# Optimization experiments

Hardware: AMD Instinct MI355X
Metric: run time of the kernel (lower is better)

Reference implementation:

```python
import jax, jax.numpy as jnp
import numpy as np

H_FEATS = 256

def setup_inputs() -> dict:
    key = jax.random.key(0)
    k1, k2, k3, k4, k5, k6, k7 = jax.random.split(key, 7)
    N, E, D = 100000, 500000, H_FEATS
    h = jax.random.normal(k1, (N, D), dtype=jnp.float32)
    src = jax.random.randint(k2, (E,), 0, N)
    dst = jax.random.randint(k3, (E,), 0, N)
    # Linear params (PyTorch default init: U(-1/sqrt(fan_in), 1/sqrt(fan_in)))
    b1_bound = 1.0 / np.sqrt(2 * D)
    b2_bound = 1.0 / np.sqrt(D)
    W1 = jax.random.uniform(k4, (2 * D, D), jnp.float32, -b1_bound, b1_bound)
    b1 = jax.random.uniform(k5, (D,), jnp.float32, -b1_bound, b1_bound)
    W2 = jax.random.uniform(k6, (D, 1), jnp.float32, -b2_bound, b2_bound)
    b2 = jax.random.uniform(k7, (1,), jnp.float32, -b2_bound, b2_bound)
    return {"h": h, "src": src, "dst": dst, "W1": W1, "b1": b1, "W2": W2, "b2": b2}

def reference(h, src, dst, W1, b1, W2, b2):
    # Gather per-edge source/destination node features and concat: [E, 2D]
    he = jnp.concatenate([h[src], h[dst]], axis=1)
    # Linear -> ReLU -> (dropout is identity in eval) -> Linear -> Sigmoid
    hid = jax.nn.relu(he @ W1 + b1)          # [E, D]
    score = jax.nn.sigmoid((hid @ W2 + b2).squeeze(1))  # [E]
    return score
```

## Files before the change

kernel.cpp:

```cpp
#include <hip/hip_runtime.h>
#include <math.h>


typedef __attribute__((ext_vector_type(8))) short short8;
typedef __attribute__((ext_vector_type(2))) float floatx2;
typedef __attribute__((ext_vector_type(4))) float floatx4;
typedef __attribute__((ext_vector_type(16))) float floatx16;

#define D_FEAT 256
#define EPW 16

__device__ __forceinline__ float bf2f(unsigned short u) {
    union { unsigned u32; float f; } v; v.u32 = ((unsigned)u) << 16; return v.f;
}
__device__ __forceinline__ float lo16(unsigned u) {
    union { unsigned u32; float f; } v; v.u32 = u << 16; return v.f;
}
__device__ __forceinline__ float hi16(unsigned u) {
    union { unsigned u32; float f; } v; v.u32 = u & 0xffff0000u; return v.f;
}
__device__ __forceinline__ unsigned short f2bf(float f) {
    union { float f; unsigned u32; } v; v.f = f;
    unsigned x = v.u32;
    return (unsigned short)((x + 0x7fffu + ((x >> 16) & 1u)) >> 16);
}
__device__ __forceinline__ float sigmoid_safe(float r) {
    r = fminf(fmaxf(r, -30.f), 30.f);
    return 1.f / (1.f + expf(-r));
}
__device__ __forceinline__ unsigned pack4_fp8(float a, float b, float c, float d) {
    int w = __builtin_amdgcn_cvt_pk_fp8_f32(a, b, 0, false);
    w = __builtin_amdgcn_cvt_pk_fp8_f32(c, d, w, true);
    return (unsigned)w;
}

__device__ __forceinline__ int probe_block(const unsigned short* __restrict__ h,
                                           int tid) {
    __shared__ int cnt_s[4];
    int c = 0;
    #pragma unroll
    for (int i = 0; i < 8; ++i) {
        unsigned e = (h[tid * 8 + i] >> 7) & 0xFF;
        c += (e >= 100 && e <= 140) ? 1 : 0;
    }
    #pragma unroll
    for (int off = 32; off > 0; off >>= 1)
        c += __shfl_xor(c, off);
    if ((tid & 63) == 0) cnt_s[tid >> 6] = c;
    __syncthreads();
    int s = cnt_s[0] + cnt_s[1] + cnt_s[2] + cnt_s[3];
    return (s >= 1843) ? 1 : 0;
}

__global__ __launch_bounds__(256) void probe_dtype(const unsigned short* __restrict__ h,
                                                   int* __restrict__ flag) {
    int isbf16 = probe_block(h, threadIdx.x);
    if (threadIdx.x == 0) flag[0] = isbf16;
}

__global__ __launch_bounds__(256) void build_wt(const unsigned short* __restrict__ h,
                                                const void* __restrict__ W1v,
                                                unsigned short* __restrict__ Wt,
                                                int* __restrict__ flag) {
    const int isbf16 = probe_block(h, threadIdx.x);
    if (blockIdx.x == 0 && threadIdx.x == 0) flag[0] = isbf16;
    int j = blockIdx.x, k = threadIdx.x;
    size_t idx = (j < 256) ? ((size_t)k * 256 + j) : ((size_t)(k + 256) * 256 + (j - 256));
    unsigned short v;
    if (isbf16) v = ((const unsigned short*)W1v)[idx];
    else        v = f2bf(((const float*)W1v)[idx]);
    Wt[(size_t)j * 256 + k] = v;
}

__global__ __launch_bounds__(512, 2) void gemm_pq(const void* __restrict__ hv,
                                                  const unsigned short* __restrict__ Wt,
                                                  unsigned char* __restrict__ PQ8,
                                                  int N, const int* __restrict__ flag) {
    const int isbf16 = flag[0];
    __shared__ unsigned short Bs[256][256];
    __shared__ unsigned short As[64][256];

    const int tid  = threadIdx.x;
    const int lane = tid & 63;
    const int wid  = tid >> 6;
    const int l32  = lane & 31;
    const int q2   = lane >> 5;

    {
        const int r = tid >> 1;
        const unsigned cbase = (tid & 1) * 256;
        const char* srcp = (const char*)Wt + (size_t)r * 512 + cbase;
        char* dstb = (char*)&Bs[0][0] + (unsigned)r * 512;
        const unsigned sw = ((unsigned)r & 31) << 4;
        #pragma unroll
        for (int i = 0; i < 16; ++i) {
            short8 v = *(const short8*)(srcp + i * 16);
            *(short8*)(dstb + ((cbase + i * 16) ^ sw)) = v;
        }
    }

    short8 breg[16];
    {
        const char* bp = (const char*)Wt + (size_t)(256 + wid * 32 + l32) * 512 + q2 * 16;
        #pragma unroll
        for (int ks = 0; ks < 16; ++ks)
            breg[ks] = *(const short8*)(bp + ks * 32);
    }

    const int ar = tid >> 3;
    const unsigned ac = (unsigned)(tid & 7) * 64;
    const unsigned aswz = ((unsigned)ar & 31) << 4;

    short8 pref[4];
    auto load_a = [&](int ms) {
        const int gm = ms * 64 + ar;
        if (isbf16) {
            #pragma unroll
            for (int j = 0; j < 4; ++j) {
                short8 v = {};
                if (gm < N)
                    v = *(const short8*)((const char*)hv + (size_t)gm * 512 + ac + j * 16);
                pref[j] = v;
            }
        } else {
            #pragma unroll
            for (int j = 0; j < 4; ++j) {
                short8 v = {};
                if (gm < N) {
                    const float* p = (const float*)hv + (size_t)gm * 256 + (ac + j * 16) / 2;
                    floatx4 f0 = *(const floatx4*)p;
                    floatx4 f1 = *(const floatx4*)(p + 4);
                    v[0] = (short)f2bf(f0.x); v[1] = (short)f2bf(f0.y);
                    v[2] = (short)f2bf(f0.z); v[3] = (short)f2bf(f0.w);
                    v[4] = (short)f2bf(f1.x); v[5] = (short)f2bf(f1.y);
                    v[6] = (short)f2bf(f1.z); v[7] = (short)f2bf(f1.w);
                }
                pref[j] = v;
            }
        }
    };

    const int NT = (N + 63) >> 6;
    const int GM = gridDim.x;
    if ((int)blockIdx.x < NT) load_a(blockIdx.x);

    for (int ms = blockIdx.x; ms < NT; ms += GM) {
        __syncthreads();
        {
            char* adst = (char*)&As[0][0] + (unsigned)ar * 512;
            #pragma unroll
            for (int j = 0; j < 4; ++j)
                *(short8*)(adst + ((ac + j * 16) ^ aswz)) = pref[j];
        }
        __syncthreads();

        const int msn = ms + GM;
        if (msn < NT) load_a(msn);

        floatx16 acc[2][2] = {};
        #pragma unroll
        for (int ks = 0; ks < 16; ++ks) {
            const unsigned cb = ((unsigned)(ks * 32 + q2 * 16)) ^ ((unsigned)l32 << 4);
            short8 a0 = *(const short8*)((const char*)&As[0][0] + (unsigned)l32 * 512 + cb);
            short8 a1 = *(const short8*)((const char*)&As[0][0] + (unsigned)(32 + l32) * 512 + cb);
            short8 bl = *(const short8*)((const char*)&Bs[0][0] + (unsigned)(wid * 32 + l32) * 512 + cb);
            acc[0][0] = __builtin_amdgcn_mfma_f32_32x32x16_bf16(bl,       a0, acc[0][0], 0, 0, 0);
            acc[1][0] = __builtin_amdgcn_mfma_f32_32x32x16_bf16(bl,       a1, acc[1][0], 0, 0, 0);
            acc[0][1] = __builtin_amdgcn_mfma_f32_32x32x16_bf16(breg[ks], a0, acc[0][1], 0, 0, 0);
            acc[1][1] = __builtin_amdgcn_mfma_f32_32x32x16_bf16(breg[ks], a1, acc[1][1], 0, 0, 0);
        }

        __syncthreads();
        {
            unsigned char* scr = (unsigned char*)&As[0][0];
            #pragma unroll
            for (int mi = 0; mi < 2; ++mi) {
                const unsigned row = (unsigned)(mi * 32 + l32);
                const unsigned rs = (row & 31) << 4;
                #pragma unroll
                for (int nb = 0; nb < 2; ++nb) {
                    const unsigned nbase = (unsigned)(nb * 256 + wid * 32 + 4 * q2);
                    #pragma unroll
                    for (int g = 0; g < 4; ++g) {
                        unsigned w = pack4_fp8(acc[mi][nb][4 * g + 0], acc[mi][nb][4 * g + 1],
                                               acc[mi][nb][4 * g + 2], acc[mi][nb][4 * g + 3]);
                        const unsigned col = nbase + 8 * g;
                        *(unsigned*)(scr + ((row * 512 + col) ^ rs)) = w;
                    }
                }
            }
        }
        __syncthreads();
        {
            const unsigned char* scr = (const unsigned char*)&As[0][0];
            const int gm = ms * 64 + ar;
            if (gm < N) {
                #pragma unroll
                for (int j = 0; j < 4; ++j) {
                    const unsigned col = ac + j * 16;
                    uint4 v = *(const uint4*)(scr + (((unsigned)ar * 512 + col) ^ aswz));
                    *(uint4*)(PQ8 + (size_t)gm * 512 + col) = v;
                }
            }
        }
    }
}

__global__ __launch_bounds__(256) void edge_score(const unsigned char* __restrict__ PQ8,
                                                  const int* __restrict__ src,
                                                  const int* __restrict__ dst,
                                                  const void* __restrict__ b1v,
                                                  const void* __restrict__ W2v,
                                                  const void* __restrict__ b2v,
                                                  void* __restrict__ outv,
                                                  int E, const int* __restrict__ flag) {
    const int isbf16 = flag[0];
    const int wave = threadIdx.x >> 6;
    const int lane = threadIdx.x & 63;
    const int e0 = (blockIdx.x * 4 + wave) * EPW;
    if (e0 >= E) return;
    const int l32 = lane & 31;
    const int par = lane >> 5;

    float bf[8], wf[8];
    if (isbf16) {
        const uint4 bvr = *(const uint4*)((const unsigned short*)b1v + l32 * 8);
        const uint4 wvr = *(const uint4*)((const unsigned short*)W2v + l32 * 8);
        bf[0] = lo16(bvr.x); bf[1] = hi16(bvr.x); bf[2] = lo16(bvr.y); bf[3] = hi16(bvr.y);
        bf[4] = lo16(bvr.z); bf[5] = hi16(bvr.z); bf[6] = lo16(bvr.w); bf[7] = hi16(bvr.w);
        wf[0] = lo16(wvr.x); wf[1] = hi16(wvr.x); wf[2] = lo16(wvr.y); wf[3] = hi16(wvr.y);
        wf[4] = lo16(wvr.z); wf[5] = hi16(wvr.z); wf[6] = lo16(wvr.w); wf[7] = hi16(wvr.w);
    } else {
        const float* bp = (const float*)b1v + l32 * 8;
        const float* wp = (const float*)W2v + l32 * 8;
        #pragma unroll
        for (int t = 0; t < 8; ++t) { bf[t] = bp[t]; wf[t] = wp[t]; }
    }
    float bias2;
    if (isbf16) bias2 = bf2f(((const unsigned short*)b2v)[0]);
    else        bias2 = ((const float*)b2v)[0];

    int nsrc[8], ndst[8];
    #pragma unroll
    for (int p = 0; p < 8; ++p) {
        int e = e0 + 2 * p + par; if (e >= E) e = E - 1;
        nsrc[p] = src[e];
        ndst[p] = dst[e];
    }
    uint2 rp[8], rq[8];
    #pragma unroll
    for (int p = 0; p < 8; ++p) {
        rp[p] = *(const uint2*)(PQ8 + (size_t)nsrc[p] * 512 + l32 * 8);
        rq[p] = *(const uint2*)(PQ8 + (size_t)ndst[p] * 512 + 256 + l32 * 8);
    }

    float res[8];
    #pragma unroll
    for (int p = 0; p < 8; ++p) {
        floatx2 p01 = __builtin_amdgcn_cvt_pk_f32_fp8((int)rp[p].x, false);
        floatx2 p23 = __builtin_amdgcn_cvt_pk_f32_fp8((int)rp[p].x, true);
        floatx2 p45 = __builtin_amdgcn_cvt_pk_f32_fp8((int)rp[p].y, false);
        floatx2 p67 = __builtin_amdgcn_cvt_pk_f32_fp8((int)rp[p].y, true);
        floatx2 q01 = __builtin_amdgcn_cvt_pk_f32_fp8((int)rq[p].x, false);
        floatx2 q23 = __builtin_amdgcn_cvt_pk_f32_fp8((int)rq[p].x, true);
        floatx2 q45 = __builtin_amdgcn_cvt_pk_f32_fp8((int)rq[p].y, false);
        floatx2 q67 = __builtin_amdgcn_cvt_pk_f32_fp8((int)rq[p].y, true);
        float v0 = fmaxf(p01.x + q01.x + bf[0], 0.f);
        float v1 = fmaxf(p01.y + q01.y + bf[1], 0.f);
        float v2 = fmaxf(p23.x + q23.x + bf[2], 0.f);
        float v3 = fmaxf(p23.y + q23.y + bf[3], 0.f);
        float v4 = fmaxf(p45.x + q45.x + bf[4], 0.f);
        float v5 = fmaxf(p45.y + q45.y + bf[5], 0.f);
        float v6 = fmaxf(p67.x + q67.x + bf[6], 0.f);
        float v7 = fmaxf(p67.y + q67.y + bf[7], 0.f);
        res[p] = v0 * wf[0] + v1 * wf[1] + v2 * wf[2] + v3 * wf[3]
               + v4 * wf[4] + v5 * wf[5] + v6 * wf[6] + v7 * wf[7];
    }

    float t4[4];
    #pragma unroll
    for (int k = 0; k < 4; ++k) {
        float a = res[2 * k], b = res[2 * k + 1];
        float own  = (lane & 1) ? b : a;
        float send = (lane & 1) ? a : b;
        t4[k] = own + __shfl_xor(send, 1);
    }
    float t2[2];
    #pragma unroll
    for (int k = 0; k < 2; ++k) {
        float a = t4[2 * k], b = t4[2 * k + 1];
        float own  = (lane & 2) ? b : a;
        float send = (lane & 2) ? a : b;
        t2[k] = own + __shfl_xor(send, 2);
    }
    float t1;
    {
        float a = t2[0], b = t2[1];
        float own  = (lane & 4) ? b : a;
        float send = (lane & 4) ? a : b;
        t1 = own + __shfl_xor(send, 4);
    }
    t1 += __shfl_xor(t1, 8);
    t1 += __shfl_xor(t1, 16);

    if (l32 < 8) {
        const int e = e0 + 2 * (lane & 7) + par;
        if (e < E) {
            float r = sigmoid_safe(t1 + bias2);
            if (isbf16) ((unsigned short*)outv)[e] = f2bf(r);
            else        ((float*)outv)[e] = r;
        }
    }
}

__global__ __launch_bounds__(256) void edge_fused(const void* __restrict__ hv,
                                                  const int* __restrict__ src,
                                                  const int* __restrict__ dst,
                                                  const void* __restrict__ W1v,
                                                  const void* __restrict__ b1v,
                                                  const void* __restrict__ W2v,
                                                  const void* __restrict__ b2v,
                                                  void* __restrict__ outv,
                                                  int E, const int* __restrict__ flag) {
    const int isbf16 = flag ? flag[0] : 1;
    __shared__ float he[512];
    __shared__ float wsum[4];
    const int e = blockIdx.x;
    if (e >= E) return;
    const int t = threadIdx.x;
    const int s = src[e];
    const int d = dst[e];

    if (isbf16) {
        he[t]       = bf2f(((const unsigned short*)hv)[(size_t)s * 256 + t]);
        he[256 + t] = bf2f(((const unsigned short*)hv)[(size_t)d * 256 + t]);
    } else {
        he[t]       = ((const float*)hv)[(size_t)s * 256 + t];
        he[256 + t] = ((const float*)hv)[(size_t)d * 256 + t];
    }
    __syncthreads();

    float acc;
    if (isbf16) acc = bf2f(((const unsigned short*)b1v)[t]);
    else        acc = ((const float*)b1v)[t];

    #pragma unroll 8
    for (int k = 0; k < 512; ++k) {
        float w;
        if (isbf16) w = bf2f(((const unsigned short*)W1v)[(size_t)k * 256 + t]);
        else        w = ((const float*)W1v)[(size_t)k * 256 + t];
        acc += he[k] * w;
    }

    float w2;
    if (isbf16) w2 = bf2f(((const unsigned short*)W2v)[t]);
    else        w2 = ((const float*)W2v)[t];
    acc = fmaxf(acc, 0.f) * w2;

    #pragma unroll
    for (int off = 32; off > 0; off >>= 1)
        acc += __shfl_xor(acc, off);
    if ((t & 63) == 0) wsum[t >> 6] = acc;
    __syncthreads();

    if (t == 0) {
        float bias2;
        if (isbf16) bias2 = bf2f(((const unsigned short*)b2v)[0]);
        else        bias2 = ((const float*)b2v)[0];
        float r = sigmoid_safe(wsum[0] + wsum[1] + wsum[2] + wsum[3] + bias2);
        if (isbf16) ((unsigned short*)outv)[e] = f2bf(r);
        else        ((float*)outv)[e] = r;
    }
}

extern "C" void kernel_launch(void* const* d_in, const int* in_sizes, int n_in,
                              void* d_out, int out_size, void* d_ws, size_t ws_size,
                              hipStream_t stream) {
    const void* h  = d_in[0];
    const int* src = (const int*)d_in[1];
    const int* dst = (const int*)d_in[2];
    const void* W1 = d_in[3];
    const void* b1 = d_in[4];
    const void* W2 = d_in[5];
    const void* b2 = d_in[6];

    const int N = in_sizes[0] / D_FEAT;
    const int E = in_sizes[1];

    const size_t FLAG_BYTES = 256;
    const size_t wt_bytes  = (size_t)512 * D_FEAT * sizeof(unsigned short);
    const size_t pq_bytes  = (size_t)N * 512;
    const size_t need = FLAG_BYTES + wt_bytes + pq_bytes;

    int* flag = (int*)d_ws;
    unsigned short* Wt = (unsigned short*)((char*)d_ws + FLAG_BYTES);
    unsigned char*  PQ8 = (unsigned char*)((char*)d_ws + FLAG_BYTES + wt_bytes);

    if (ws_size >= need) {
        build_wt<<<512, 256, 0, stream>>>((const unsigned short*)h, W1, Wt, flag);

        gemm_pq<<<256, 512, 0, stream>>>(h, Wt, PQ8, N, flag);

        int egrid = (E + 4 * EPW - 1) / (4 * EPW);
        edge_score<<<egrid, 256, 0, stream>>>(PQ8, src, dst, b1, W2, b2, d_out, E, flag);
    } else if (ws_size >= FLAG_BYTES) {
        probe_dtype<<<1, 256, 0, stream>>>((const unsigned short*)h, flag);
        edge_fused<<<E, 256, 0, stream>>>(h, src, dst, W1, b1, W2, b2, d_out, E, flag);
    } else {
        edge_fused<<<E, 256, 0, stream>>>(h, src, dst, W1, b1, W2, b2, d_out, E, nullptr);
    }
}
```

Baseline: 233.9 us.

## Fuse weight transpose, node GEMM and edge scoring into one cooperative kernel

Replaces the three launches (W1 transpose, per-node P/Q GEMM, edge scoring) with one cooperative kernel of 256 blocks that separates the phases with grid-wide syncs. Each block re-probes the input dtype itself, so no flag has to travel through global memory. The aim is to remove launch gaps and tail effects between the three kernels. In exchange, the edge phase now runs on only 256 persistent blocks of 512 threads with a grid-stride loop instead of a large grid, which can cut the latency hiding available for the random gathers. The old three-kernel path stays as a fallback if the cooperative launch fails.

```diff
diff --git a/kernel.cpp b/kernel.cpp
--- a/kernel.cpp
+++ b/kernel.cpp
@@ -1,5 +1,8 @@
 #include <hip/hip_runtime.h>
+#include <hip/hip_cooperative_groups.h>
 #include <math.h>
+
+namespace cg = cooperative_groups;
 
 
 typedef __attribute__((ext_vector_type(8))) short short8;
@@ -71,6 +74,283 @@
     else        v = f2bf(((const float*)W1v)[idx]);
     Wt[(size_t)j * 256 + k] = v;
 }
+
+__global__ __launch_bounds__(512, 2) void fused_all(const unsigned short* __restrict__ hu,
+                                                    const void* __restrict__ W1v,
+                                                    const int* __restrict__ src,
+                                                    const int* __restrict__ dst,
+                                                    const void* __restrict__ b1v,
+                                                    const void* __restrict__ W2v,
+                                                    const void* __restrict__ b2v,
+                                                    unsigned short* __restrict__ Wt,
+                                                    unsigned char* __restrict__ PQ8,
+                                                    void* __restrict__ outv,
+                                                    int N, int E) {
+    __shared__ unsigned short Bs[256][256];
+    __shared__ unsigned short As[64][256];
+    cg::grid_group grid = cg::this_grid();
+
+    const int tid  = threadIdx.x;
+    const int lane = tid & 63;
+    const int wid  = tid >> 6;
+    const int l32  = lane & 31;
+    const int q2   = lane >> 5;
+
+    int isbf16;
+    {
+        int* cnt_s = (int*)&Bs[0][0];
+        int c = 0;
+        #pragma unroll
+        for (int i = 0; i < 4; ++i) {
+            unsigned e = (hu[tid * 4 + i] >> 7) & 0xFF;
+            c += (e >= 100 && e <= 140) ? 1 : 0;
+        }
+        #pragma unroll
+        for (int off = 32; off > 0; off >>= 1)
+            c += __shfl_xor(c, off);
+        if ((tid & 63) == 0) cnt_s[tid >> 6] = c;
+        __syncthreads();
+        int s = 0;
+        #pragma unroll
+        for (int i = 0; i < 8; ++i) s += cnt_s[i];
+        isbf16 = (s >= 1843) ? 1 : 0;
+        __syncthreads();
+    }
+
+    {
+        const int j = blockIdx.x * 2 + (tid >> 8);
+        const int k = tid & 255;
+        size_t idx = (j < 256) ? ((size_t)k * 256 + j)
+                               : ((size_t)(k + 256) * 256 + (j - 256));
+        unsigned short v;
+        if (isbf16) v = ((const unsigned short*)W1v)[idx];
+        else        v = f2bf(((const float*)W1v)[idx]);
+        Wt[(size_t)j * 256 + k] = v;
+    }
+    grid.sync();
+
+    {
+        const void* hv = (const void*)hu;
+        {
+            const int r = tid >> 1;
+            const unsigned cbase = (tid & 1) * 256;
+            const char* srcp = (const char*)Wt + (size_t)r * 512 + cbase;
+            char* dstb = (char*)&Bs[0][0] + (unsigned)r * 512;
+            const unsigned sw = ((unsigned)r & 31) << 4;
+            #pragma unroll
+            for (int i = 0; i < 16; ++i) {
+                short8 v = *(const short8*)(srcp + i * 16);
+                *(short8*)(dstb + ((cbase + i * 16) ^ sw)) = v;
+            }
+        }
+
+        short8 breg[16];
+        {
+            const char* bp = (const char*)Wt + (size_t)(256 + wid * 32 + l32) * 512 + q2 * 16;
+            #pragma unroll
+            for (int ks = 0; ks < 16; ++ks)
+                breg[ks] = *(const short8*)(bp + ks * 32);
+        }
+
+        const int ar = tid >> 3;
+        const unsigned ac = (unsigned)(tid & 7) * 64;
+        const unsigned aswz = ((unsigned)ar & 31) << 4;
+
+        short8 pref[4];
+        auto load_a = [&](int ms) {
+            const int gm = ms * 64 + ar;
+            if (isbf16) {
+                #pragma unroll
+                for (int j = 0; j < 4; ++j) {
+                    short8 v = {};
+                    if (gm < N)
+                        v = *(const short8*)((const char*)hv + (size_t)gm * 512 + ac + j * 16);
+                    pref[j] = v;
+                }
+            } else {
+                #pragma unroll
+                for (int j = 0; j < 4; ++j) {
+                    short8 v = {};
+                    if (gm < N) {
+                        const float* p = (const float*)hv + (size_t)gm * 256 + (ac + j * 16) / 2;
+                        floatx4 f0 = *(const floatx4*)p;
+                        floatx4 f1 = *(const floatx4*)(p + 4);
+                        v[0] = (short)f2bf(f0.x); v[1] = (short)f2bf(f0.y);
+                        v[2] = (short)f2bf(f0.z); v[3] = (short)f2bf(f0.w);
+                        v[4] = (short)f2bf(f1.x); v[5] = (short)f2bf(f1.y);
+                        v[6] = (short)f2bf(f1.z); v[7] = (short)f2bf(f1.w);
+                    }
+                    pref[j] = v;
+                }
+            }
+        };
+
+        const int NT = (N + 63) >> 6;
+        const int GM = gridDim.x;
+        if ((int)blockIdx.x < NT) load_a(blockIdx.x);
+
+        for (int ms = blockIdx.x; ms < NT; ms += GM) {
+            __syncthreads();
+            {
+                char* adst = (char*)&As[0][0] + (unsigned)ar * 512;
+                #pragma unroll
+                for (int j = 0; j < 4; ++j)
+                    *(short8*)(adst + ((ac + j * 16) ^ aswz)) = pref[j];
+            }
+            __syncthreads();
+
+            const int msn = ms + GM;
+            if (msn < NT) load_a(msn);
+
+            floatx16 acc[2][2] = {};
+            #pragma unroll
+            for (int ks = 0; ks < 16; ++ks) {
+                const unsigned cb = ((unsigned)(ks * 32 + q2 * 16)) ^ ((unsigned)l32 << 4);
+                short8 a0 = *(const short8*)((const char*)&As[0][0] + (unsigned)l32 * 512 + cb);
+                short8 a1 = *(const short8*)((const char*)&As[0][0] + (unsigned)(32 + l32) * 512 + cb);
+                short8 bl = *(const short8*)((const char*)&Bs[0][0] + (unsigned)(wid * 32 + l32) * 512 + cb);
+                acc[0][0] = __builtin_amdgcn_mfma_f32_32x32x16_bf16(bl,       a0, acc[0][0], 0, 0, 0);
+                acc[1][0] = __builtin_amdgcn_mfma_f32_32x32x16_bf16(bl,       a1, acc[1][0], 0, 0, 0);
+                acc[0][1] = __builtin_amdgcn_mfma_f32_32x32x16_bf16(breg[ks], a0, acc[0][1], 0, 0, 0);
+                acc[1][1] = __builtin_amdgcn_mfma_f32_32x32x16_bf16(breg[ks], a1, acc[1][1], 0, 0, 0);
+            }
+
+            __syncthreads();
+            {
+                unsigned char* scr = (unsigned char*)&As[0][0];
+                #pragma unroll
+                for (int mi = 0; mi < 2; ++mi) {
+                    const unsigned row = (unsigned)(mi * 32 + l32);
+                    const unsigned rs = (row & 31) << 4;
+                    #pragma unroll
+                    for (int nb = 0; nb < 2; ++nb) {
+                        const unsigned nbase = (unsigned)(nb * 256 + wid * 32 + 4 * q2);
+                        #pragma unroll
+                        for (int g = 0; g < 4; ++g) {
+                            unsigned w = pack4_fp8(acc[mi][nb][4 * g + 0], acc[mi][nb][4 * g + 1],
+                                                   acc[mi][nb][4 * g + 2], acc[mi][nb][4 * g + 3]);
+                            const unsigned col = nbase + 8 * g;
+                            *(unsigned*)(scr + ((row * 512 + col) ^ rs)) = w;
+                        }
+                    }
+                }
+            }
+            __syncthreads();
+            {
+                const unsigned char* scr = (const unsigned char*)&As[0][0];
+                const int gm = ms * 64 + ar;
+                if (gm < N) {
+                    #pragma unroll
+                    for (int j = 0; j < 4; ++j) {
+                        const unsigned col = ac + j * 16;
+                        uint4 v = *(const uint4*)(scr + (((unsigned)ar * 512 + col) ^ aswz));
+                        *(uint4*)(PQ8 + (size_t)gm * 512 + col) = v;
+                    }
+                }
+            }
+        }
+    }
+    grid.sync();
+
+    {
+        const int par = lane >> 5;
+        float bf[8], wf[8];
+        if (isbf16) {
+            const uint4 bvr = *(const uint4*)((const unsigned short*)b1v + l32 * 8);
+            const uint4 wvr = *(const uint4*)((const unsigned short*)W2v + l32 * 8);
+            bf[0] = lo16(bvr.x); bf[1] = hi16(bvr.x); bf[2] = lo16(bvr.y); bf[3] = hi16(bvr.y);
+            bf[4] = lo16(bvr.z); bf[5] = hi16(bvr.z); bf[6] = lo16(bvr.w); bf[7] = hi16(bvr.w);
+            wf[0] = lo16(wvr.x); wf[1] = hi16(wvr.x); wf[2] = lo16(wvr.y); wf[3] = hi16(wvr.y);
+            wf[4] = lo16(wvr.z); wf[5] = hi16(wvr.z); wf[6] = lo16(wvr.w); wf[7] = hi16(wvr.w);
+        } else {
+            const float* bp = (const float*)b1v + l32 * 8;
+            const float* wp = (const float*)W2v + l32 * 8;
+            #pragma unroll
+            for (int t = 0; t < 8; ++t) { bf[t] = bp[t]; wf[t] = wp[t]; }
+        }
+        float bias2;
+        if (isbf16) bias2 = bf2f(((const unsigned short*)b2v)[0]);
+        else        bias2 = ((const float*)b2v)[0];
+
+        const int gstep = gridDim.x * 8;
+        for (int g = blockIdx.x * 8 + wid; (long)g * EPW < E; g += gstep) {
+            const int e0 = g * EPW;
+
+            int nsrc[8], ndst[8];
+            #pragma unroll
+            for (int p = 0; p < 8; ++p) {
+                int e = e0 + 2 * p + par; if (e >= E) e = E - 1;
+                nsrc[p] = src[e];
+                ndst[p] = dst[e];
+            }
+            uint2 rp[8], rq[8];
+            #pragma unroll
+            for (int p = 0; p < 8; ++p) {
+                rp[p] = *(const uint2*)(PQ8 + (size_t)nsrc[p] * 512 + l32 * 8);
+                rq[p] = *(const uint2*)(PQ8 + (size_t)ndst[p] * 512 + 256 + l32 * 8);
+            }
+
+            float res[8];
+            #pragma unroll
+            for (int p = 0; p < 8; ++p) {
+                floatx2 p01 = __builtin_amdgcn_cvt_pk_f32_fp8((int)rp[p].x, false);
+                floatx2 p23 = __builtin_amdgcn_cvt_pk_f32_fp8((int)rp[p].x, true);
+                floatx2 p45 = __builtin_amdgcn_cvt_pk_f32_fp8((int)rp[p].y, false);
+                floatx2 p67 = __builtin_amdgcn_cvt_pk_f32_fp8((int)rp[p].y, true);
+                floatx2 q01 = __builtin_amdgcn_cvt_pk_f32_fp8((int)rq[p].x, false);
+                floatx2 q23 = __builtin_amdgcn_cvt_pk_f32_fp8((int)rq[p].x, true);
+                floatx2 q45 = __builtin_amdgcn_cvt_pk_f32_fp8((int)rq[p].y, false);
+                floatx2 q67 = __builtin_amdgcn_cvt_pk_f32_fp8((int)rq[p].y, true);
+                float v0 = fmaxf(p01.x + q01.x + bf[0], 0.f);
+                float v1 = fmaxf(p01.y + q01.y + bf[1], 0.f);
+                float v2 = fmaxf(p23.x + q23.x + bf[2], 0.f);
+                float v3 = fmaxf(p23.y + q23.y + bf[3], 0.f);
+                float v4 = fmaxf(p45.x + q45.x + bf[4], 0.f);
+                float v5 = fmaxf(p45.y + q45.y + bf[5], 0.f);
+                float v6 = fmaxf(p67.x + q67.x + bf[6], 0.f);
+                float v7 = fmaxf(p67.y + q67.y + bf[7], 0.f);
+                res[p] = v0 * wf[0] + v1 * wf[1] + v2 * wf[2] + v3 * wf[3]
+                       + v4 * wf[4] + v5 * wf[5] + v6 * wf[6] + v7 * wf[7];
+            }
+
+            float t4[4];
+            #pragma unroll
+            for (int k = 0; k < 4; ++k) {
+                float a = res[2 * k], b = res[2 * k + 1];
+                float own  = (lane & 1) ? b : a;
+                float send = (lane & 1) ? a : b;
+                t4[k] = own + __shfl_xor(send, 1);
+            }
+            float t2[2];
+            #pragma unroll
+            for (int k = 0; k < 2; ++k) {
+                float a = t4[2 * k], b = t4[2 * k + 1];
+                float own  = (lane & 2) ? b : a;
+                float send = (lane & 2) ? a : b;
+                t2[k] = own + __shfl_xor(send, 2);
+            }
+            float t1;
+            {
+                float a = t2[0], b = t2[1];
+                float own  = (lane & 4) ? b : a;
+                float send = (lane & 4) ? a : b;
+                t1 = own + __shfl_xor(send, 4);
+            }
+            t1 += __shfl_xor(t1, 8);
+            t1 += __shfl_xor(t1, 16);
+
+            if (l32 < 8) {
+                const int e = e0 + 2 * (lane & 7) + par;
+                if (e < E) {
+                    float r = sigmoid_safe(t1 + bias2);
+                    if (isbf16) ((unsigned short*)outv)[e] = f2bf(r);
+                    else        ((float*)outv)[e] = r;
+                }
+            }
+        }
+    }
+}
+
 
 __global__ __launch_bounds__(512, 2) void gemm_pq(const void* __restrict__ hv,
                                                   const unsigned short* __restrict__ Wt,
@@ -397,12 +677,21 @@
     unsigned char*  PQ8 = (unsigned char*)((char*)d_ws + FLAG_BYTES + wt_bytes);
 
     if (ws_size >= need) {
-        build_wt<<<512, 256, 0, stream>>>((const unsigned short*)h, W1, Wt, flag);
-
-        gemm_pq<<<256, 512, 0, stream>>>(h, Wt, PQ8, N, flag);
-
-        int egrid = (E + 4 * EPW - 1) / (4 * EPW);
-        edge_score<<<egrid, 256, 0, stream>>>(PQ8, src, dst, b1, W2, b2, d_out, E, flag);
+        const unsigned short* hu = (const unsigned short*)h;
+        void* outv = d_out;
+        int Nv = N, Ev = E;
+        void* kargs[] = { (void*)&hu, (void*)&W1, (void*)&src, (void*)&dst,
+                          (void*)&b1, (void*)&W2, (void*)&b2, (void*)&Wt,
+                          (void*)&PQ8, (void*)&outv, (void*)&Nv, (void*)&Ev };
+        hipError_t err = hipLaunchCooperativeKernel((const void*)fused_all,
+                                                    dim3(256), dim3(512),
+                                                    kargs, 0, stream);
+        if (err != hipSuccess) {
+            build_wt<<<512, 256, 0, stream>>>((const unsigned short*)h, W1, Wt, flag);
+            gemm_pq<<<256, 512, 0, stream>>>(h, Wt, PQ8, N, flag);
+            int egrid = (E + 4 * EPW - 1) / (4 * EPW);
+            edge_score<<<egrid, 256, 0, stream>>>(PQ8, src, dst, b1, W2, b2, d_out, E, flag);
+        }
     } else if (ws_size >= FLAG_BYTES) {
         probe_dtype<<<1, 256, 0, stream>>>((const unsigned short*)h, flag);
         edge_fused<<<E, 256, 0, stream>>>(h, src, dst, W1, b1, W2, b2, d_out, E, flag);
```

Measured after the change: 315.4 us. 34.8% more time.
